# Optimization experiments

Measured on AMD Instinct MI355X. Metric: run time of the kernel, lower is better.

Reference implementation:

```python
import jax, jax.numpy as jnp
import numpy as np

N_NODES = 100000
N_EDGES = 1600000
D = 64


def setup_inputs() -> dict:
    key = jax.random.key(0)
    k1, k2, k3, k4, k5 = jax.random.split(key, 5)
    h = jax.random.normal(k1, (N_NODES, D), dtype=jnp.float32)
    edge_src = jax.random.randint(k2, (N_EDGES,), 0, N_NODES, dtype=jnp.int32)
    edge_dst = jax.random.randint(k3, (N_EDGES,), 0, N_NODES, dtype=jnp.int32)
    # nn.Linear(D, D) params (kaiming-ish scale)
    W = jax.random.normal(k4, (D, D), dtype=jnp.float32) / np.sqrt(D)
    b = jax.random.normal(k5, (D,), dtype=jnp.float32) * 0.01
    return {"h": h, "edge_src": edge_src, "edge_dst": edge_dst, "W": W, "b": b}


def reference(h, edge_src, edge_dst, W, b):
    # Linear projection on node features: [N, D] @ [D, D]^T + b (torch Linear convention)
    h2 = h @ W.T + b
    # copy_u + mean: per-dst mean of src features over incoming edges.
    msgs = h2[edge_src]                                             # [E, D] gather
    summed = jax.ops.segment_sum(msgs, edge_dst, num_segments=N_NODES)  # [N, D] scatter-add
    deg = jax.ops.segment_sum(jnp.ones_like(edge_dst, dtype=h.dtype), edge_dst,
                              num_segments=N_NODES)                 # [N]
    # DGL mean leaves zero-in-degree nodes at 0; guard divide-by-zero.
    agg = summed / jnp.maximum(deg, 1.0)[:, None]
    return jax.nn.relu(agg)
```

## Files before the change

kernel.cpp:

```cpp
#include <hip/hip_runtime.h>

#define D 64
#define LOCB 6
#define BWN  (1 << LOCB)
#define MAXB 2048
#define PBLK 64

typedef __attribute__((ext_vector_type(8))) short bf16x8;
typedef __attribute__((ext_vector_type(4))) float f32x4;

__device__ __forceinline__ unsigned short f2bf(float x) {
    unsigned int u = __float_as_uint(x);
    u += 0x7FFFu + ((u >> 16) & 1u);
    return (unsigned short)(u >> 16);
}

__global__ __launch_bounds__(256) void cvt_kernel(
    const float4* __restrict__ h4, ushort4* __restrict__ hb4, int nh4,
    const float4* __restrict__ W4, ushort4* __restrict__ Wb4, int nw4)
{
    const int tid = blockIdx.x * blockDim.x + threadIdx.x;
    const int gsz = gridDim.x * blockDim.x;
    for (int i = tid; i < nw4; i += gsz) {
        const float4 f = W4[i];
        ushort4 o;
        o.x = f2bf(f.x); o.y = f2bf(f.y); o.z = f2bf(f.z); o.w = f2bf(f.w);
        Wb4[i] = o;
    }
    for (int i = tid; i < nh4; i += gsz) {
        const float4 f = h4[i];
        ushort4 o;
        o.x = f2bf(f.x); o.y = f2bf(f.y); o.z = f2bf(f.z); o.w = f2bf(f.w);
        hb4[i] = o;
    }
}

__global__ __launch_bounds__(1024) void part_kernel(
    const int* __restrict__ esrc, const int* __restrict__ edst,
    int* __restrict__ bcnt, int* __restrict__ bpair,
    int NBK, int CAPM, int E, int PCHUNK)
{
    __shared__ int hist[MAXB];
    __shared__ int basep[MAXB];
    __shared__ int cur[MAXB];

    const int tid    = threadIdx.x;
    const int base_e = blockIdx.x * PCHUNK;
    const int cnt_e  = min(PCHUNK, E - base_e);
    if (cnt_e <= 0) return;

    for (int k = tid; k < NBK; k += 1024) { hist[k] = 0; cur[k] = 0; }
    __syncthreads();

    const int4* ed4 = (const int4*)(edst + base_e);
    const int4* es4 = (const int4*)(esrc + base_e);
    const int n4 = cnt_e >> 2;

    for (int i = tid; i < n4; i += 1024) {
        const int4 d = ed4[i];
        atomicAdd(&hist[d.x >> LOCB], 1);
        atomicAdd(&hist[d.y >> LOCB], 1);
        atomicAdd(&hist[d.z >> LOCB], 1);
        atomicAdd(&hist[d.w >> LOCB], 1);
    }
    if (tid == 0)
        for (int e = base_e + (cnt_e & ~3); e < base_e + cnt_e; ++e)
            atomicAdd(&hist[edst[e] >> LOCB], 1);
    __syncthreads();

    for (int k = tid; k < NBK; k += 1024) {
        const int c = hist[k];
        if (c > 0) basep[k] = atomicAdd(&bcnt[k], c);
    }
    __syncthreads();

    for (int i = tid; i < n4; i += 1024) {
        const int4 s = es4[i];
        const int4 d = ed4[i];
        int bk, p;
        bk = d.x >> LOCB; p = basep[bk] + atomicAdd(&cur[bk], 1);
        if (p < CAPM) bpair[(size_t)bk * CAPM + p] = (s.x << LOCB) | (d.x & (BWN - 1));
        bk = d.y >> LOCB; p = basep[bk] + atomicAdd(&cur[bk], 1);
        if (p < CAPM) bpair[(size_t)bk * CAPM + p] = (s.y << LOCB) | (d.y & (BWN - 1));
        bk = d.z >> LOCB; p = basep[bk] + atomicAdd(&cur[bk], 1);
        if (p < CAPM) bpair[(size_t)bk * CAPM + p] = (s.z << LOCB) | (d.z & (BWN - 1));
        bk = d.w >> LOCB; p = basep[bk] + atomicAdd(&cur[bk], 1);
        if (p < CAPM) bpair[(size_t)bk * CAPM + p] = (s.w << LOCB) | (d.w & (BWN - 1));
    }
    if (tid == 0)
        for (int e = base_e + (cnt_e & ~3); e < base_e + cnt_e; ++e) {
            const int bk = edst[e] >> LOCB;
            const int p = basep[bk] + atomicAdd(&cur[bk], 1);
            if (p < CAPM)
                bpair[(size_t)bk * CAPM + p] = (esrc[e] << LOCB) | (edst[e] & (BWN - 1));
        }
}

template <bool HB16>
__global__ __launch_bounds__(256) void mega_kernel(
    const void* __restrict__ hsrc,
    const int* __restrict__ bcnt, const int* __restrict__ bpair, int CAPM,
    const unsigned short* __restrict__ Wb,
    const float* __restrict__ bias,
    float* __restrict__ out, int N)
{
    constexpr int GW   = HB16 ? 8 : 16;
    constexpr int FPL  = HB16 ? 8 : 4;
    constexpr int MAXCH = 64 / GW;
    constexpr int NGRP = 64 / GW;
    constexpr int PASSES = (BWN / 4) / NGRP;

    __shared__ int ellcnt[BWN];
    __shared__ int ell[BWN][65];
    __shared__ unsigned short ms[BWN * D];

    const int tid  = threadIdx.x;
    const int w    = tid >> 6;
    const int lane = tid & 63;
    const int bkt  = blockIdx.x;
    const int node0 = bkt << LOCB;

    for (int i = tid; i < BWN; i += 256) ellcnt[i] = 0;
    __syncthreads();

    const int nE = min(bcnt[bkt], CAPM);
    for (int i = tid; i < nE; i += 256) {
        const int e   = bpair[(size_t)bkt * CAPM + i];
        const int loc = e & (BWN - 1);
        const int src = e >> LOCB;
        const int p = atomicAdd(&ellcnt[loc], 1);
        if (p < 64) ell[loc][p] = src;
    }
    __syncthreads();

    const int g  = lane / GW;
    const int gl = lane % GW;
    const unsigned short* __restrict__ hb = (const unsigned short*)hsrc;
    const float*          __restrict__ hf = (const float*)hsrc;

    #pragma unroll
    for (int ps = 0; ps < PASSES; ++ps) {
        const int loc  = w * (BWN / 4) + ps * NGRP + g;
        const int degT = ellcnt[loc];
        const int deg  = min(degT, 64);

        float a[FPL];
        #pragma unroll
        for (int i = 0; i < FPL; ++i) a[i] = 0.f;

        #pragma unroll
        for (int c = 0; c < MAXCH; ++c) {
            if (c * GW < deg) {
                const int sl  = ell[loc][c * GW + gl];
                const int rem = deg - c * GW;
                #pragma unroll
                for (int j = 0; j < GW; ++j) {
                    if (j < rem) {
                        const int s = __shfl(sl, j, GW);
                        if constexpr (HB16) {
                            const int4 v = *(const int4*)(hb + (size_t)s * D + gl * 8);
                            a[0] += __uint_as_float((unsigned)v.x << 16);
                            a[1] += __uint_as_float((unsigned)v.x & 0xffff0000u);
                            a[2] += __uint_as_float((unsigned)v.y << 16);
                            a[3] += __uint_as_float((unsigned)v.y & 0xffff0000u);
                            a[4] += __uint_as_float((unsigned)v.z << 16);
                            a[5] += __uint_as_float((unsigned)v.z & 0xffff0000u);
                            a[6] += __uint_as_float((unsigned)v.w << 16);
                            a[7] += __uint_as_float((unsigned)v.w & 0xffff0000u);
                        } else {
                            const float4 v = *(const float4*)(hf + (size_t)s * D + gl * 4);
                            a[0] += v.x; a[1] += v.y; a[2] += v.z; a[3] += v.w;
                        }
                    }
                }
            }
        }

        const float inv = (degT > 0) ? 1.f / (float)degT : 0.f;
        #pragma unroll
        for (int i = 0; i < FPL; ++i) a[i] *= inv;

        char* msb = (char*)ms;
        if constexpr (HB16) {
            int4 o;
            o.x = (int)(((unsigned)f2bf(a[1]) << 16) | f2bf(a[0]));
            o.y = (int)(((unsigned)f2bf(a[3]) << 16) | f2bf(a[2]));
            o.z = (int)(((unsigned)f2bf(a[5]) << 16) | f2bf(a[4]));
            o.w = (int)(((unsigned)f2bf(a[7]) << 16) | f2bf(a[6]));
            *(int4*)(msb + loc * 128 + ((gl * 16) ^ ((loc & 7) << 4))) = o;
        } else {
            int2 o;
            o.x = (int)(((unsigned)f2bf(a[1]) << 16) | f2bf(a[0]));
            o.y = (int)(((unsigned)f2bf(a[3]) << 16) | f2bf(a[2]));
            *(int2*)(msb + loc * 128 + ((gl * 8) ^ ((loc & 7) << 4))) = o;
        }
    }
    __syncthreads();

    const int r16 = lane & 15;
    const int kq  = lane >> 4;
    const int rl0 = w * 16;
    bf16x8 afr[2];
    #pragma unroll
    for (int ks = 0; ks < 2; ++ks) {
        const int row = rl0 + r16;
        afr[ks] = *(const bf16x8*)((char*)ms + row * 128 +
                    ((ks * 64 + kq * 16) ^ ((row & 7) << 4)));
    }
    int dmask[4];
    #pragma unroll
    for (int r = 0; r < 4; ++r) dmask[r] = ellcnt[rl0 + kq * 4 + r];

    #pragma unroll
    for (int cb = 0; cb < 4; ++cb) {
        const unsigned short* wp = Wb + (size_t)(cb * 16 + r16) * D + kq * 8;
        const bf16x8 b0 = *(const bf16x8*)wp;
        const bf16x8 b1 = *(const bf16x8*)(wp + 32);
        f32x4 acc = {0.f, 0.f, 0.f, 0.f};
        acc = __builtin_amdgcn_mfma_f32_16x16x32_bf16(afr[0], b0, acc, 0, 0, 0);
        acc = __builtin_amdgcn_mfma_f32_16x16x32_bf16(afr[1], b1, acc, 0, 0, 0);

        const float bb = bias[cb * 16 + r16];
        #pragma unroll
        for (int r = 0; r < 4; ++r) {
            const int node = node0 + rl0 + kq * 4 + r;
            if (node < N) {
                const float val = acc[r] + bb;
                out[(size_t)node * D + cb * 16 + r16] =
                    (dmask[r] > 0) ? fmaxf(val, 0.f) : 0.f;
            }
        }
    }
}

extern "C" void kernel_launch(void* const* d_in, const int* in_sizes, int n_in,
                              void* d_out, int out_size, void* d_ws, size_t ws_size,
                              hipStream_t stream) {
    const float* h    = (const float*)d_in[0];
    const int*   esrc = (const int*)d_in[1];
    const int*   edst = (const int*)d_in[2];
    const float* W    = (const float*)d_in[3];
    const float* b    = (const float*)d_in[4];

    const int N = in_sizes[0] / D;
    const int E = in_sizes[1];

    float* out = (float*)d_out;

    const int NBK  = (N + BWN - 1) >> LOCB;
    const int CAPM = 1792;
    const int PCHUNK = (E + PBLK - 1) / PBLK;

    const size_t padB  = (size_t)((NBK + 63) & ~63) * 4;
    const size_t pairB = (size_t)NBK * CAPM * 4;
    const size_t wbB   = (size_t)D * D * 2;
    const size_t hbB   = (size_t)N * D * 2;
    const bool HB = (ws_size >= padB + pairB + wbB + hbB);

    int*            bcnt  = (int*)d_ws;
    int*            bpair = bcnt + ((NBK + 63) & ~63);
    unsigned short* Wb    = (unsigned short*)(bpair + (size_t)NBK * CAPM);
    unsigned short* hb    = Wb + (size_t)D * D;

    hipMemsetAsync(bcnt, 0, (size_t)NBK * sizeof(int), stream);

    cvt_kernel<<<2048, 256, 0, stream>>>(
        (const float4*)h, (ushort4*)hb, HB ? N * D / 4 : 0,
        (const float4*)W, (ushort4*)Wb, D * D / 4);

    part_kernel<<<PBLK, 1024, 0, stream>>>(
        esrc, edst, bcnt, bpair, NBK, CAPM, E, PCHUNK);

    if (HB)
        mega_kernel<true><<<NBK, 256, 0, stream>>>(
            hb, bcnt, bpair, CAPM, Wb, b, out, N);
    else
        mega_kernel<false><<<NBK, 256, 0, stream>>>(
            h, bcnt, bpair, CAPM, Wb, b, out, N);
}
```

Baseline: 177.8 us.

## Aggregate via LDS float atomics instead of ELL gather; fold memset into cvt

Replaces the per-bucket ELL construction plus per-node gather with a direct edge-parallel scatter: each 8-lane group loads one source row and atomically adds it into an fp32 shared accumulator, counting degree with shared atomics. This removes the ELL-building phase, a barrier, and the load imbalance from varying in-degree, at the cost of many LDS atomic adds per edge and a larger shared tile. It also zeroes the bucket counters inside the conversion kernel to drop a separate memset, and doubles the partition block count.

```diff
diff --git a/kernel.cpp b/kernel.cpp
--- a/kernel.cpp
+++ b/kernel.cpp
@@ -4,7 +4,9 @@
 #define LOCB 6
 #define BWN  (1 << LOCB)
 #define MAXB 2048
-#define PBLK 64
+#define PBLK 128
+#define CAPM 1792
+#define MSP  68
 
 typedef __attribute__((ext_vector_type(8))) short bf16x8;
 typedef __attribute__((ext_vector_type(4))) float f32x4;
@@ -17,10 +19,12 @@
 
 __global__ __launch_bounds__(256) void cvt_kernel(
     const float4* __restrict__ h4, ushort4* __restrict__ hb4, int nh4,
-    const float4* __restrict__ W4, ushort4* __restrict__ Wb4, int nw4)
+    const float4* __restrict__ W4, ushort4* __restrict__ Wb4, int nw4,
+    int* __restrict__ bcnt, int nbk)
 {
     const int tid = blockIdx.x * blockDim.x + threadIdx.x;
     const int gsz = gridDim.x * blockDim.x;
+    for (int i = tid; i < nbk; i += gsz) bcnt[i] = 0;
     for (int i = tid; i < nw4; i += gsz) {
         const float4 f = W4[i];
         ushort4 o;
@@ -38,7 +42,7 @@
 __global__ __launch_bounds__(1024) void part_kernel(
     const int* __restrict__ esrc, const int* __restrict__ edst,
     int* __restrict__ bcnt, int* __restrict__ bpair,
-    int NBK, int CAPM, int E, int PCHUNK)
+    int NBK, int E, int PCHUNK)
 {
     __shared__ int hist[MAXB];
     __shared__ int basep[MAXB];
@@ -99,20 +103,16 @@
 template <bool HB16>
 __global__ __launch_bounds__(256) void mega_kernel(
     const void* __restrict__ hsrc,
-    const int* __restrict__ bcnt, const int* __restrict__ bpair, int CAPM,
+    const int* __restrict__ bcnt, const int* __restrict__ bpair,
     const unsigned short* __restrict__ Wb,
     const float* __restrict__ bias,
     float* __restrict__ out, int N)
 {
-    constexpr int GW   = HB16 ? 8 : 16;
-    constexpr int FPL  = HB16 ? 8 : 4;
-    constexpr int MAXCH = 64 / GW;
-    constexpr int NGRP = 64 / GW;
-    constexpr int PASSES = (BWN / 4) / NGRP;
-
-    __shared__ int ellcnt[BWN];
-    __shared__ int ell[BWN][65];
-    __shared__ unsigned short ms[BWN * D];
+    constexpr int GW  = HB16 ? 8 : 16;
+    constexpr int EPW = 64 / GW;
+
+    __shared__ float ms[BWN][MSP];
+    __shared__ int   cntS[BWN];
 
     const int tid  = threadIdx.x;
     const int w    = tid >> 6;
@@ -120,79 +120,45 @@
     const int bkt  = blockIdx.x;
     const int node0 = bkt << LOCB;
 
-    for (int i = tid; i < BWN; i += 256) ellcnt[i] = 0;
+    float* msf = &ms[0][0];
+    for (int i = tid; i < BWN * MSP; i += 256) msf[i] = 0.f;
+    for (int i = tid; i < BWN; i += 256) cntS[i] = 0;
     __syncthreads();
 
     const int nE = min(bcnt[bkt], CAPM);
-    for (int i = tid; i < nE; i += 256) {
-        const int e   = bpair[(size_t)bkt * CAPM + i];
-        const int loc = e & (BWN - 1);
-        const int src = e >> LOCB;
-        const int p = atomicAdd(&ellcnt[loc], 1);
-        if (p < 64) ell[loc][p] = src;
-    }
-    __syncthreads();
+    const int* bp = bpair + (size_t)bkt * CAPM;
 
     const int g  = lane / GW;
     const int gl = lane % GW;
     const unsigned short* __restrict__ hb = (const unsigned short*)hsrc;
     const float*          __restrict__ hf = (const float*)hsrc;
 
-    #pragma unroll
-    for (int ps = 0; ps < PASSES; ++ps) {
-        const int loc  = w * (BWN / 4) + ps * NGRP + g;
-        const int degT = ellcnt[loc];
-        const int deg  = min(degT, 64);
-
-        float a[FPL];
-        #pragma unroll
-        for (int i = 0; i < FPL; ++i) a[i] = 0.f;
-
-        #pragma unroll
-        for (int c = 0; c < MAXCH; ++c) {
-            if (c * GW < deg) {
-                const int sl  = ell[loc][c * GW + gl];
-                const int rem = deg - c * GW;
-                #pragma unroll
-                for (int j = 0; j < GW; ++j) {
-                    if (j < rem) {
-                        const int s = __shfl(sl, j, GW);
-                        if constexpr (HB16) {
-                            const int4 v = *(const int4*)(hb + (size_t)s * D + gl * 8);
-                            a[0] += __uint_as_float((unsigned)v.x << 16);
-                            a[1] += __uint_as_float((unsigned)v.x & 0xffff0000u);
-                            a[2] += __uint_as_float((unsigned)v.y << 16);
-                            a[3] += __uint_as_float((unsigned)v.y & 0xffff0000u);
-                            a[4] += __uint_as_float((unsigned)v.z << 16);
-                            a[5] += __uint_as_float((unsigned)v.z & 0xffff0000u);
-                            a[6] += __uint_as_float((unsigned)v.w << 16);
-                            a[7] += __uint_as_float((unsigned)v.w & 0xffff0000u);
-                        } else {
-                            const float4 v = *(const float4*)(hf + (size_t)s * D + gl * 4);
-                            a[0] += v.x; a[1] += v.y; a[2] += v.z; a[3] += v.w;
-                        }
-                    }
-                }
+    for (int i0 = w * EPW; i0 < nE; i0 += 4 * EPW) {
+        const int idx = i0 + g;
+        if (idx < nE) {
+            const int e   = bp[idx];
+            const int loc = e & (BWN - 1);
+            const int src = e >> LOCB;
+            if constexpr (HB16) {
+                const int4 v = *(const int4*)(hb + (size_t)src * D + gl * 8);
+                float* mrow = &ms[loc][gl * 8];
+                atomicAdd(&mrow[0], __uint_as_float((unsigned)v.x << 16));
+                atomicAdd(&mrow[1], __uint_as_float((unsigned)v.x & 0xffff0000u));
+                atomicAdd(&mrow[2], __uint_as_float((unsigned)v.y << 16));
+                atomicAdd(&mrow[3], __uint_as_float((unsigned)v.y & 0xffff0000u));
+                atomicAdd(&mrow[4], __uint_as_float((unsigned)v.z << 16));
+                atomicAdd(&mrow[5], __uint_as_float((unsigned)v.z & 0xffff0000u));
+                atomicAdd(&mrow[6], __uint_as_float((unsigned)v.w << 16));
+                atomicAdd(&mrow[7], __uint_as_float((unsigned)v.w & 0xffff0000u));
+            } else {
+                const float4 v = *(const float4*)(hf + (size_t)src * D + gl * 4);
+                float* mrow = &ms[loc][gl * 4];
+                atomicAdd(&mrow[0], v.x);
+                atomicAdd(&mrow[1], v.y);
+                atomicAdd(&mrow[2], v.z);
+                atomicAdd(&mrow[3], v.w);
             }
-        }
-
-        const float inv = (degT > 0) ? 1.f / (float)degT : 0.f;
-        #pragma unroll
-        for (int i = 0; i < FPL; ++i) a[i] *= inv;
-
-        char* msb = (char*)ms;
-        if constexpr (HB16) {
-            int4 o;
-            o.x = (int)(((unsigned)f2bf(a[1]) << 16) | f2bf(a[0]));
-            o.y = (int)(((unsigned)f2bf(a[3]) << 16) | f2bf(a[2]));
-            o.z = (int)(((unsigned)f2bf(a[5]) << 16) | f2bf(a[4]));
-            o.w = (int)(((unsigned)f2bf(a[7]) << 16) | f2bf(a[6]));
-            *(int4*)(msb + loc * 128 + ((gl * 16) ^ ((loc & 7) << 4))) = o;
-        } else {
-            int2 o;
-            o.x = (int)(((unsigned)f2bf(a[1]) << 16) | f2bf(a[0]));
-            o.y = (int)(((unsigned)f2bf(a[3]) << 16) | f2bf(a[2]));
-            *(int2*)(msb + loc * 128 + ((gl * 8) ^ ((loc & 7) << 4))) = o;
+            if (gl == 0) atomicAdd(&cntS[loc], 1);
         }
     }
     __syncthreads();
@@ -200,16 +166,28 @@
     const int r16 = lane & 15;
     const int kq  = lane >> 4;
     const int rl0 = w * 16;
+    const int row = rl0 + r16;
+
+    const int dgA = cntS[row];
+    const float invA = (dgA > 0) ? 1.f / (float)dgA : 0.f;
+
     bf16x8 afr[2];
     #pragma unroll
     for (int ks = 0; ks < 2; ++ks) {
-        const int row = rl0 + r16;
-        afr[ks] = *(const bf16x8*)((char*)ms + row * 128 +
-                    ((ks * 64 + kq * 16) ^ ((row & 7) << 4)));
-    }
+        const float* mp = &ms[row][ks * 32 + kq * 8];
+        const float4 f0 = *(const float4*)mp;
+        const float4 f1 = *(const float4*)(mp + 4);
+        bf16x8 a;
+        a[0] = (short)f2bf(f0.x * invA); a[1] = (short)f2bf(f0.y * invA);
+        a[2] = (short)f2bf(f0.z * invA); a[3] = (short)f2bf(f0.w * invA);
+        a[4] = (short)f2bf(f1.x * invA); a[5] = (short)f2bf(f1.y * invA);
+        a[6] = (short)f2bf(f1.z * invA); a[7] = (short)f2bf(f1.w * invA);
+        afr[ks] = a;
+    }
+
     int dmask[4];
     #pragma unroll
-    for (int r = 0; r < 4; ++r) dmask[r] = ellcnt[rl0 + kq * 4 + r];
+    for (int r = 0; r < 4; ++r) dmask[r] = cntS[rl0 + kq * 4 + r];
 
     #pragma unroll
     for (int cb = 0; cb < 4; ++cb) {
@@ -247,8 +225,7 @@
 
     float* out = (float*)d_out;
 
-    const int NBK  = (N + BWN - 1) >> LOCB;
-    const int CAPM = 1792;
+    const int NBK    = (N + BWN - 1) >> LOCB;
     const int PCHUNK = (E + PBLK - 1) / PBLK;
 
     const size_t padB  = (size_t)((NBK + 63) & ~63) * 4;
@@ -262,19 +239,18 @@
     unsigned short* Wb    = (unsigned short*)(bpair + (size_t)NBK * CAPM);
     unsigned short* hb    = Wb + (size_t)D * D;
 
-    hipMemsetAsync(bcnt, 0, (size_t)NBK * sizeof(int), stream);
-
     cvt_kernel<<<2048, 256, 0, stream>>>(
         (const float4*)h, (ushort4*)hb, HB ? N * D / 4 : 0,
-        (const float4*)W, (ushort4*)Wb, D * D / 4);
+        (const float4*)W, (ushort4*)Wb, D * D / 4,
+        bcnt, NBK);
 
     part_kernel<<<PBLK, 1024, 0, stream>>>(
-        esrc, edst, bcnt, bpair, NBK, CAPM, E, PCHUNK);
+        esrc, edst, bcnt, bpair, NBK, E, PCHUNK);
 
     if (HB)
         mega_kernel<true><<<NBK, 256, 0, stream>>>(
-            hb, bcnt, bpair, CAPM, Wb, b, out, N);
+            hb, bcnt, bpair, Wb, b, out, N);
     else
         mega_kernel<false><<<NBK, 256, 0, stream>>>(
-            h, bcnt, bpair, CAPM, Wb, b, out, N);
-}
+            h, bcnt, bpair, Wb, b, out, N);
+}
```

After: 701.6 us. +294.7%, slower.
